# Kernel tuning notes

Hardware: AMD Instinct MI355X
Metric: run time of the kernel (lower is better)

## Reference

```python
import jax, jax.numpy as jnp
import numpy as np

jax.config.update("jax_enable_x64", True)  # scipy.special.expi computes in float64; match it internally

_GAMMA = 0.5772156649015328606  # Euler-Mascheroni constant
_SERIES_TERMS = 120   # power series: accurate for |x| <= 40 in float64
_ASYM_TERMS = 30      # asymptotic series for x >= 40
_CF_DEPTH = 60        # continued fraction for E1(z), z >= 6
_X_HI = 40.0
_X_LO = -6.0


def _ei_series(x):
    # Ei(x) = gamma + ln|x| + sum_{n>=1} x^n / (n * n!)
    def body(carry, n):
        t, s = carry
        t = t * x / n          # t_n = x^n / n!
        return (t, s + t / n), None
    ns = jnp.arange(1.0, _SERIES_TERMS + 1.0, dtype=x.dtype)
    (_, s), _ = jax.lax.scan(body, (jnp.ones_like(x), jnp.zeros_like(x)), ns)
    return _GAMMA + jnp.log(jnp.abs(x)) + s


def _ei_asymptotic(x):
    # Ei(x) ~ e^x / x * sum_{k>=0} k! / x^k   (x large positive)
    def body(carry, k):
        t, s = carry
        t = t * k / x          # t_k = k! / x^k
        return (t, s + t), None
    ks = jnp.arange(1.0, _ASYM_TERMS + 1.0, dtype=x.dtype)
    (_, s), _ = jax.lax.scan(body, (jnp.ones_like(x), jnp.ones_like(x)), ks)
    return jnp.exp(x) / x * s


def _e1_cf(z):
    # E1(z) = e^{-z} / (z + 1 - 1/(z + 3 - 4/(z + 5 - 9/(...))))  (z > 0)
    def body(i, f):
        k = _CF_DEPTH - i      # k runs _CF_DEPTH .. 1
        return z + 2.0 * k - 1.0 - (k * k) / f
    f0 = z + 2.0 * _CF_DEPTH + 1.0
    f = jax.lax.fori_loop(0, _CF_DEPTH, body, f0)
    return jnp.exp(-z) / f


def _ei_impl(x):
    xs = x.astype(jnp.float64)
    ser = _ei_series(jnp.clip(xs, _X_LO, _X_HI))
    asy = _ei_asymptotic(jnp.maximum(xs, _X_HI))
    neg = -_e1_cf(jnp.maximum(-xs, -_X_LO))   # Ei(x) = -E1(-x) for x < 0
    out = jnp.where(xs >= _X_HI, asy, jnp.where(xs <= _X_LO, neg, ser))
    return out.astype(x.dtype)


@jax.custom_vjp
def ei(x):
    return _ei_impl(x)


def _ei_fwd(x):
    return _ei_impl(x), x


def _ei_bwd(x, g):
    # matches the torch module's custom backward: d/dx Ei(x) = e^x / x
    return (g * jnp.exp(x) / x,)


ei.defvjp(_ei_fwd, _ei_bwd)


def setup_inputs() -> dict:
    key = jax.random.key(0)
    # scale by 20 so all three Ei domains (series / neg continued fraction / asymptotic) are hit
    x = jax.random.normal(key, (8192, 4096), dtype=jnp.float32) * 20.0
    return {"x": x}


def reference(x):
    return ei(x)
```

## Files before the change

kernel.cpp:

```cpp
#include <hip/hip_runtime.h>
#include <math.h>


static constexpr double cexp(double x) {
    double t = x * 1.4426950408889634074;
    long long n = (long long)(t + (t >= 0 ? 0.5 : -0.5));
    double r = x - (double)n * 0.693147180559945286227e0;
    r -= (double)n * 2.319046813846299558e-17;
    double s = 1.0, term = 1.0;
    for (int k = 1; k <= 22; ++k) { term = term * r / (double)k; s += term; }
    double p = 1.0, b = 2.0;
    long long m = n < 0 ? -n : n;
    while (m) { if (m & 1) p *= b; b *= b; m >>= 1; }
    return n < 0 ? s / p : s * p;
}
static constexpr double clog(double x) {
    int e = 0; double m = x;
    while (m > 1.4142135623730951) { m *= 0.5; ++e; }
    while (m < 0.7071067811865476) { m *= 2.0; --e; }
    double t = (m - 1.0) / (m + 1.0), t2 = t * t, s = 0.0, p = t;
    for (int k = 0; k < 14; ++k) { s += p / (double)(2 * k + 1); p *= t2; }
    return 2.0 * s + (double)e * 0.69314718055994530942;
}
static constexpr double f_value(double x) {
    if (x <= -6.0) {
        double z = -x;
        double f = z + 121.0;
        for (int k = 60; k >= 1; --k)
            f = z + 2.0 * (double)k - 1.0 - ((double)k * (double)k) / f;
        return -1.0 / f;
    } else if (x >= 40.0) {
        double u = 1.0 / x, s = 1.0, t = 1.0;
        for (int k = 1; k <= 30; ++k) { t = t * (double)k * u; s += t; }
        return u * s;
    } else {
        double t = 1.0, s = 0.0;
        for (int n = 1; n <= 120; ++n) { t = t * x / (double)n; s += t / (double)n; }
        double Ei = 0.57721566490153286061 + clog(x < 0.0 ? -x : x) + s;
        return Ei * cexp(-x);
    }
}
static constexpr double S_coeff(double x, int k) {
    double sum = 0.0, nf = 1.0;
    for (int n = 1; n <= 45; ++n) {
        nf *= (double)n;
        if (n >= k) {
            double c = 1.0;
            for (int t = 0; t < k; ++t) c = c * (double)(n - t) / (double)(t + 1);
            double xp = 1.0;
            for (int t = 0; t < n - k; ++t) xp *= x;
            sum += c * xp / ((double)n * nf);
        }
    }
    return sum;
}

struct Chunk { alignas(16) float c[256][4]; };
static constexpr Chunk make_chunk(int base) {
    Chunk ch{};
    for (int i = 0; i < 256; ++i) {
        double xj = -128.0 + 0.0625 * (double)(base + i);
        if (xj > -0.95 && xj < 0.95) {
            for (int k = 0; k < 4; ++k) ch.c[i][k] = (float)S_coeff(xj, k);
        } else {
            double fk = f_value(xj);
            ch.c[i][0] = (float)fk;
            double fact = 1.0, xp = 1.0, kf = 1.0;
            for (int k = 1; k <= 3; ++k) {
                if (k >= 2) fact *= (double)(k - 1);
                xp *= xj;
                fk = ((k & 1) ? fact : -fact) / xp - fk;
                kf *= (double)k;
                ch.c[i][k] = (float)(fk / kf);
            }
        }
    }
    return ch;
}
static constexpr Chunk g_c0  = make_chunk(0);    static constexpr Chunk g_c1  = make_chunk(256);
static constexpr Chunk g_c2  = make_chunk(512);  static constexpr Chunk g_c3  = make_chunk(768);
static constexpr Chunk g_c4  = make_chunk(1024); static constexpr Chunk g_c5  = make_chunk(1280);
static constexpr Chunk g_c6  = make_chunk(1536); static constexpr Chunk g_c7  = make_chunk(1792);
static constexpr Chunk g_c8  = make_chunk(2048); static constexpr Chunk g_c9  = make_chunk(2304);
static constexpr Chunk g_c10 = make_chunk(2560); static constexpr Chunk g_c11 = make_chunk(2816);
static constexpr Chunk g_c12 = make_chunk(3072); static constexpr Chunk g_c13 = make_chunk(3328);
static constexpr Chunk g_c14 = make_chunk(3584); static constexpr Chunk g_c15 = make_chunk(3840);
__device__ const Chunk g_tab[16] = {g_c0,g_c1,g_c2,g_c3,g_c4,g_c5,g_c6,g_c7,
                                    g_c8,g_c9,g_c10,g_c11,g_c12,g_c13,g_c14,g_c15};

__device__ __forceinline__ float ei_one(float xf) {
    int j = (int)rintf(fmaf(xf, 16.0f, 2048.0f));
    j = j < 0 ? 0 : (j > 4095 ? 4095 : j);
    const float* cp = g_tab[j >> 8].c[j & 255];
    float4 c = *(const float4*)cp;
    float xj = fmaf(0.0625f, (float)j, -128.0f);
    float d = xf - xj;
    float s = fmaf(fmaf(fmaf(c.w, d, c.z), d, c.y), d, c.x);
    float nf = rintf(xf * 1.44269504f);
    float rr = fmaf(nf, -0.693145751953125f, xf);
    rr = fmaf(nf, -1.42860677e-6f, rr);
    float E = ldexpf(exp2f(rr * 1.44269504f), (int)nf);
    float rA = E * s;
    float rB = fmaf(0.69314718f, log2f(fabsf(xf)), 0.57721566f) + s;
    float r = (j > 2032 && j < 2064) ? rB : rA;
    if (!(r == r)) r = 0.0f;
    return fminf(fmaxf(r, -3.3e38f), 3.3e38f);
}

__global__ __launch_bounds__(256)
void ei_kernel(const float* __restrict__ x, float* __restrict__ out, int n) {
    int i = blockIdx.x * blockDim.x + threadIdx.x;
    int base = i * 4;
    if (base + 3 < n) {
        float4 xv = *(const float4*)(x + base);
        float4 o;
        o.x = ei_one(xv.x);
        o.y = ei_one(xv.y);
        o.z = ei_one(xv.z);
        o.w = ei_one(xv.w);
        *(float4*)(out + base) = o;
    } else {
        for (int t = base; t < n; ++t) out[t] = ei_one(x[t]);
    }
}

extern "C" void kernel_launch(void* const* d_in, const int* in_sizes, int n_in,
                              void* d_out, int out_size, void* d_ws, size_t ws_size,
                              hipStream_t stream) {
    const float* x = (const float*)d_in[0];
    float* out = (float*)d_out;
    int n = in_sizes[0];
    int n4 = (n + 3) / 4;
    const int block = 256;
    const int grid = (n4 + block - 1) / block;
    ei_kernel<<<grid, block, 0, stream>>>(x, out, n);
}
```

Before: 259.7 us.

## Stage coefficient table in LDS with persistent grid-stride kernel

Each block copies the full 64 KB coefficient table from global memory into shared memory once, then looks up coefficients from LDS instead of doing scattered global or L2 reads. The launch changes to a fixed grid of 512 blocks of 1024 threads that walk the data with a grid-stride loop, which spreads the cost of the table copy over many elements. The exp scaling is also reordered so the ldexp is applied after the multiply by s. The trade-off is 64 KB of LDS per block, which limits occupancy, plus possible LDS bank conflicts on the random-index lookups.

```diff
diff --git a/kernel.cpp b/kernel.cpp
--- a/kernel.cpp
+++ b/kernel.cpp
@@ -88,39 +88,46 @@
 __device__ const Chunk g_tab[16] = {g_c0,g_c1,g_c2,g_c3,g_c4,g_c5,g_c6,g_c7,
                                     g_c8,g_c9,g_c10,g_c11,g_c12,g_c13,g_c14,g_c15};
 
-__device__ __forceinline__ float ei_one(float xf) {
+__device__ __forceinline__ float ei_one(float xf, const float4* s_tab) {
     int j = (int)rintf(fmaf(xf, 16.0f, 2048.0f));
     j = j < 0 ? 0 : (j > 4095 ? 4095 : j);
-    const float* cp = g_tab[j >> 8].c[j & 255];
-    float4 c = *(const float4*)cp;
+    float4 c = s_tab[j];
     float xj = fmaf(0.0625f, (float)j, -128.0f);
     float d = xf - xj;
     float s = fmaf(fmaf(fmaf(c.w, d, c.z), d, c.y), d, c.x);
     float nf = rintf(xf * 1.44269504f);
     float rr = fmaf(nf, -0.693145751953125f, xf);
     rr = fmaf(nf, -1.42860677e-6f, rr);
-    float E = ldexpf(exp2f(rr * 1.44269504f), (int)nf);
-    float rA = E * s;
+    float rA = ldexpf(exp2f(rr * 1.44269504f) * s, (int)nf);
     float rB = fmaf(0.69314718f, log2f(fabsf(xf)), 0.57721566f) + s;
     float r = (j > 2032 && j < 2064) ? rB : rA;
     if (!(r == r)) r = 0.0f;
     return fminf(fmaxf(r, -3.3e38f), 3.3e38f);
 }
 
-__global__ __launch_bounds__(256)
+__global__ __launch_bounds__(1024)
 void ei_kernel(const float* __restrict__ x, float* __restrict__ out, int n) {
-    int i = blockIdx.x * blockDim.x + threadIdx.x;
-    int base = i * 4;
-    if (base + 3 < n) {
+    __shared__ float4 s_tab[4096];
+    const float4* gt = (const float4*)g_tab;
+    #pragma unroll
+    for (int t = 0; t < 4; ++t)
+        s_tab[threadIdx.x + 1024 * t] = gt[threadIdx.x + 1024 * t];
+    __syncthreads();
+
+    int n4 = n >> 2;
+    int stride = gridDim.x * blockDim.x;
+    for (int q = blockIdx.x * blockDim.x + threadIdx.x; q < n4; q += stride) {
+        int base = q * 4;
         float4 xv = *(const float4*)(x + base);
         float4 o;
-        o.x = ei_one(xv.x);
-        o.y = ei_one(xv.y);
-        o.z = ei_one(xv.z);
-        o.w = ei_one(xv.w);
+        o.x = ei_one(xv.x, s_tab);
+        o.y = ei_one(xv.y, s_tab);
+        o.z = ei_one(xv.z, s_tab);
+        o.w = ei_one(xv.w, s_tab);
         *(float4*)(out + base) = o;
-    } else {
-        for (int t = base; t < n; ++t) out[t] = ei_one(x[t]);
+    }
+    if (blockIdx.x == 0 && threadIdx.x == 0) {
+        for (int t = n & ~3; t < n; ++t) out[t] = ei_one(x[t], s_tab);
     }
 }
 
@@ -130,8 +137,7 @@
     const float* x = (const float*)d_in[0];
     float* out = (float*)d_out;
     int n = in_sizes[0];
-    int n4 = (n + 3) / 4;
-    const int block = 256;
-    const int grid = (n4 + block - 1) / block;
+    const int block = 1024;
+    const int grid = 512;
     ei_kernel<<<grid, block, 0, stream>>>(x, out, n);
 }
```

Result: faster. 231.2 us (-11.0%).
